# Optimization experiments

Hardware: AMD Instinct MI355X
Metric: run time of the kernel (lower is better)

The kernel has to match this reference:

```python
import jax, jax.numpy as jnp
import numpy as np

B, CQ, CKV, H, W = 4, 128, 256, 64, 64
NUM_HEADS = 8
SCALE = (CQ // NUM_HEADS) ** (-0.5)


def setup_inputs() -> dict:
    key = jax.random.key(0)
    ks = jax.random.split(key, 10)
    s = 0.02
    return {
        "x_q": jax.random.normal(ks[0], (B, CQ, H, W), dtype=jnp.float32),
        "x_kv": jax.random.normal(ks[1], (B, CKV, H, W), dtype=jnp.float32),
        "Wq": jax.random.normal(ks[2], (CQ, CQ), dtype=jnp.float32) * s,
        "bq": jnp.zeros((CQ,), dtype=jnp.float32),
        "Wk": jax.random.normal(ks[3], (CQ, CKV), dtype=jnp.float32) * s,
        "bk": jnp.zeros((CQ,), dtype=jnp.float32),
        "Wv": jax.random.normal(ks[4], (CQ, CKV), dtype=jnp.float32) * s,
        "bv": jnp.zeros((CQ,), dtype=jnp.float32),
        "Wo": jax.random.normal(ks[5], (CQ, CQ), dtype=jnp.float32) * s,
        "bo": jnp.zeros((CQ,), dtype=jnp.float32),
    }


def _conv1x1(x, Wm, bv_):
    # 1x1 conv == channel-mixing matmul: [B,C,H,W] x [O,C] -> [B,O,H,W]
    return jnp.einsum('bchw,oc->bohw', x, Wm) + bv_[:, None, None]


def reference(x_q, x_kv, Wq, bq, Wk, bk, Wv, bv, Wo, bo):
    b, c, h, w = x_q.shape
    n = h * w
    Q = _conv1x1(x_q, Wq, bq).reshape(b, c, n)   # [B,C,N]
    K = _conv1x1(x_kv, Wk, bk).reshape(b, c, n)  # [B,C,N]
    V = _conv1x1(x_kv, Wv, bv).reshape(b, c, n)  # [B,C,N]
    # attn = softmax(Q^T K * scale) over keys: [B,N,N]
    attn = jax.nn.softmax(jnp.einsum('bcn,bcm->bnm', Q, K) * SCALE, axis=-1)
    out = jnp.einsum('bnm,bcm->bcn', attn, V).reshape(b, c, h, w)
    out = _conv1x1(out, Wo, bo) + x_q
    return out
```

## Files before the change

### kernel.cpp

```cpp
#include <hip/hip_runtime.h>
#include <hip/hip_bf16.h>

typedef __bf16 bf16x8 __attribute__((ext_vector_type(8)));
typedef float f32x4 __attribute__((ext_vector_type(4)));
typedef float f32x16 __attribute__((ext_vector_type(16)));

#define MFMA16(a, b, c) __builtin_amdgcn_mfma_f32_16x16x32_bf16(a, b, c, 0, 0, 0)
#define MFMA32(a, b, c) __builtin_amdgcn_mfma_f32_32x32x16_bf16(a, b, c, 0, 0, 0)

static constexpr int NSP = 4096;
static constexpr float SCALE_L2E = 0.25f * 1.4426950408889634f;

__device__ __forceinline__ bf16x8 ld_frag(const void* p) {
  int4 v = *(const int4*)p;
  return __builtin_bit_cast(bf16x8, v);
}

__device__ __forceinline__ unsigned pk2(float a, float b) {
  unsigned short x = __builtin_bit_cast(unsigned short, (__bf16)a);
  unsigned short y = __builtin_bit_cast(unsigned short, (__bf16)b);
  return (unsigned)x | ((unsigned)y << 16);
}

__device__ __forceinline__ void load_lds16(const void* g, void* l) {
  __builtin_amdgcn_global_load_lds(
      (const __attribute__((address_space(1))) unsigned*)g,
      (__attribute__((address_space(3))) unsigned*)l, 16, 0, 0);
}

__global__ void k_prep(const float* __restrict__ Wq, const float* __restrict__ bq,
                       const float* __restrict__ Wk, const float* __restrict__ Wv,
                       const float* __restrict__ Wo,
                       __bf16* __restrict__ wqb, __bf16* __restrict__ wkb,
                       __bf16* __restrict__ wvb, __bf16* __restrict__ wob,
                       float* __restrict__ bqs) {
  int i = blockIdx.x * 256 + threadIdx.x;
  if (i < 16384)      wqb[i]          = (__bf16)(Wq[i] * SCALE_L2E);
  else if (i < 49152) wkb[i - 16384]  = (__bf16)Wk[i - 16384];
  else if (i < 81920) wvb[i - 49152]  = (__bf16)Wv[i - 49152];
  else if (i < 98304) wob[i - 81920]  = (__bf16)Wo[i - 81920];
  if (i < 128) bqs[i] = bq[i] * SCALE_L2E;
}

template <bool SWZ>
__device__ __forceinline__ void store_tile_T(char* myt, const f32x4* acc, int g, int r,
                                             __bf16* dst_base) {
#pragma unroll
  for (int oc = 0; oc < 8; ++oc) {
#pragma unroll
    for (int rr = 0; rr < 4; ++rr) {
      int o = oc * 16 + g * 4 + rr;
      int byte = (r << 8) + (o << 1);
      byte ^= (r & 7) << 4;
      *(__bf16*)(myt + byte) = (__bf16)acc[oc][rr];
    }
  }
  int l = g * 16 + r;
#pragma unroll
  for (int p = 0; p < 4; ++p) {
    int u = p * 64 + l, row = u >> 4, seg = u & 15;
    int byte = (row << 8) + (seg << 4);
    if (!SWZ) byte ^= (row & 7) << 4;
    int4 v = *(int4*)(myt + byte);
    *(int4*)(dst_base + row * 128 + seg * 8) = v;
  }
}

__global__ __launch_bounds__(256) void k_proj(const float* __restrict__ xq,
                                              const float* __restrict__ xkv,
                                              const __bf16* __restrict__ wqb,
                                              const __bf16* __restrict__ wkb,
                                              const __bf16* __restrict__ wvb,
                                              const float* __restrict__ bqs,
                                              const float* __restrict__ bk,
                                              const float* __restrict__ bv,
                                              __bf16* __restrict__ Qt,
                                              __bf16* __restrict__ Kt,
                                              __bf16* __restrict__ Vm) {
  const int t = threadIdx.x, w = t >> 6, l = t & 63, r = l & 15, g = l >> 4;
  __shared__ __align__(16) char lds[16384];
  char* myt = lds + (w << 12);

  if (blockIdx.x < 256) {
    const int b = blockIdx.x >> 6;
    const int n0 = (blockIdx.x & 63) << 6;
    const int nl = n0 + (w << 4) + r;
    const float* xb = xq + ((size_t)b << 19);
    bf16x8 bx[4];
#pragma unroll
    for (int cc = 0; cc < 4; ++cc) {
#pragma unroll
      for (int i = 0; i < 8; ++i) {
        int c = cc * 32 + g * 8 + i;
        bx[cc][i] = (__bf16)xb[c * 4096 + nl];
      }
    }
    f32x4 acc[8];
#pragma unroll
    for (int oc = 0; oc < 8; ++oc)
#pragma unroll
      for (int rr = 0; rr < 4; ++rr) acc[oc][rr] = bqs[oc * 16 + g * 4 + rr];
#pragma unroll
    for (int oc = 0; oc < 8; ++oc) {
#pragma unroll
      for (int cc = 0; cc < 4; ++cc) {
        bf16x8 a = ld_frag(wqb + (oc * 16 + r) * 128 + cc * 32 + g * 8);
        acc[oc] = MFMA16(a, bx[cc], acc[oc]);
      }
    }
    store_tile_T<false>(myt, acc, g, r, Qt + ((size_t)(b * NSP + n0 + w * 16)) * 128);
  } else {
    const int bid = blockIdx.x - 256;
    const int b = bid >> 6;
    const int n0 = (bid & 63) << 6;
    const int nl = n0 + (w << 4) + r;
    const float* xb = xkv + ((size_t)b << 20);
    bf16x8 bx[8];
#pragma unroll
    for (int cc = 0; cc < 8; ++cc) {
#pragma unroll
      for (int i = 0; i < 8; ++i) {
        int c = cc * 32 + g * 8 + i;
        bx[cc][i] = (__bf16)xb[(size_t)c * 4096 + nl];
      }
    }
    f32x4 acc[8];
#pragma unroll
    for (int oc = 0; oc < 8; ++oc)
#pragma unroll
      for (int rr = 0; rr < 4; ++rr) acc[oc][rr] = bk[oc * 16 + g * 4 + rr];
#pragma unroll
    for (int oc = 0; oc < 8; ++oc) {
#pragma unroll
      for (int cc = 0; cc < 8; ++cc) {
        bf16x8 a = ld_frag(wkb + (oc * 16 + r) * 256 + cc * 32 + g * 8);
        acc[oc] = MFMA16(a, bx[cc], acc[oc]);
      }
    }
    store_tile_T<true>(myt, acc, g, r, Kt + ((size_t)(b * NSP + n0 + w * 16)) * 128);

    f32x4 av[8];
#pragma unroll
    for (int oc = 0; oc < 8; ++oc)
#pragma unroll
      for (int rr = 0; rr < 4; ++rr) av[oc][rr] = bv[oc * 16 + g * 4 + rr];
#pragma unroll
    for (int oc = 0; oc < 8; ++oc) {
#pragma unroll
      for (int cc = 0; cc < 8; ++cc) {
        bf16x8 a = ld_frag(wvb + (oc * 16 + r) * 256 + cc * 32 + g * 8);
        av[oc] = MFMA16(a, bx[cc], av[oc]);
      }
    }
#pragma unroll
    for (int oc = 0; oc < 8; ++oc) {
#pragma unroll
      for (int rr = 0; rr < 4; ++rr) {
        int o = oc * 16 + g * 4 + rr;
        Vm[((size_t)(b * 128 + o) << 12) + (nl ^ ((o & 3) << 3))] = (__bf16)av[oc][rr];
      }
    }
  }
}

template <int SPLIT>
__global__ __launch_bounds__(256, 3) void k_flash(const __bf16* __restrict__ Qt,
                                                  const __bf16* __restrict__ Kt,
                                                  const __bf16* __restrict__ Vm,
                                                  __bf16* __restrict__ Op,
                                                  float2* __restrict__ Ml) {
  const int bid = blockIdx.x;
  const int combo = bid & (4 * SPLIT - 1), qtile = bid / (4 * SPLIT);
  const int b = combo & 3, ks = combo >> 2;
  const int q0 = qtile << 7;
  const int NK = NSP / SPLIT;
  const int t = threadIdx.x, w = t >> 6, l = t & 63;
  const int q31 = l & 31, hi = l >> 5;
  const int swz = (q31 & 7) << 4;
  const int swzV = (q31 & 3) << 4;

  __shared__ __align__(16) char kl[2][8192];
  __shared__ __align__(16) char vl[2][8192];

  const int qA = q0 + w * 32 + q31;
  const __bf16* qp = Qt + ((size_t)(b * NSP + qA)) * 128;
  bf16x8 qf[8];
#pragma unroll
  for (int cc = 0; cc < 8; ++cc) qf[cc] = ld_frag(qp + cc * 16 + hi * 8);

  f32x16 acc[4];
#pragma unroll
  for (int c = 0; c < 4; ++c)
#pragma unroll
    for (int i = 0; i < 16; ++i) acc[c][i] = 0.f;
  f32x4 lp = (f32x4){0.f, 0.f, 0.f, 0.f};

  const char* kbase = (const char*)(Kt + ((size_t)(b * NSP) + ks * NK) * 128);
  const char* vbase = (const char*)(Vm + (size_t)b * 128 * NSP + ks * NK);

  auto STAGE = [&](int bi, int tt) {
#pragma unroll
    for (int i = 0; i < 2; ++i) {
      int u = i * 256 + t;
      load_lds16(kbase + tt * 8192 + u * 16, &kl[bi][u * 16]);
    }
#pragma unroll
    for (int i = 0; i < 2; ++i) {
      int u = i * 256 + t, ch = u >> 2, ko = u & 3;
      load_lds16(vbase + (size_t)ch * 8192 + tt * 64 + ko * 16, &vl[bi][u * 16]);
    }
  };

  STAGE(0, 0);
  __syncthreads();

  const int nit = NK / 32;
  for (int it = 0; it < nit; ++it) {
    const int cur = it & 1;
    if (it + 1 < nit) STAGE(cur ^ 1, it + 1);

    const char* kt = kl[cur];
    f32x16 s = {};
    __builtin_amdgcn_s_setprio(1);
#pragma unroll
    for (int cc = 0; cc < 8; ++cc) {
      bf16x8 kf = ld_frag(kt + (q31 << 8) + ((cc * 32 + hi * 16) ^ swz));
      s = MFMA32(kf, qf[cc], s);
    }
    __builtin_amdgcn_s_setprio(0);

#pragma unroll
    for (int i = 0; i < 16; ++i) s[i] = exp2f(s[i]);
#pragma unroll
    for (int i = 0; i < 16; ++i) lp[i & 3] += s[i];

    unsigned pA[4][2], rA[4][2];
#pragma unroll
    for (int q4 = 0; q4 < 4; ++q4) {
      pA[q4][0] = pk2(s[4 * q4 + 0], s[4 * q4 + 1]);
      pA[q4][1] = pk2(s[4 * q4 + 2], s[4 * q4 + 3]);
    }
#pragma unroll
    for (int q4 = 0; q4 < 4; ++q4) {
      rA[q4][0] = __shfl_xor(pA[q4][0], 32);
      rA[q4][1] = __shfl_xor(pA[q4][1], 32);
    }

    const char* vt = vl[cur];
    __builtin_amdgcn_s_setprio(1);
#pragma unroll
    for (int kb = 0; kb < 2; ++kb) {
      uint4 fa;
      fa.x = hi ? rA[2 * kb + 1][0] : pA[2 * kb][0];
      fa.y = hi ? rA[2 * kb + 1][1] : pA[2 * kb][1];
      fa.z = hi ? pA[2 * kb + 1][0] : rA[2 * kb][0];
      fa.w = hi ? pA[2 * kb + 1][1] : rA[2 * kb][1];
      bf16x8 pf = __builtin_bit_cast(bf16x8, fa);
#pragma unroll
      for (int cht = 0; cht < 4; ++cht) {
        bf16x8 vf = ld_frag(vt + (cht * 32 + q31) * 64 + ((kb * 32 + hi * 16) ^ swzV));
        acc[cht] = MFMA32(vf, pf, acc[cht]);
      }
    }
    __builtin_amdgcn_s_setprio(0);
    __syncthreads();
  }

  float lsum = (lp[0] + lp[1]) + (lp[2] + lp[3]);
  lsum += __shfl_xor(lsum, 32);

  const size_t rowA = (size_t)((ks * 4 + b) * NSP + qA) * 128;
#pragma unroll
  for (int cht = 0; cht < 4; ++cht) {
#pragma unroll
    for (int qq = 0; qq < 4; ++qq) {
      uint2 va;
      va.x = pk2(acc[cht][4 * qq + 0], acc[cht][4 * qq + 1]);
      va.y = pk2(acc[cht][4 * qq + 2], acc[cht][4 * qq + 3]);
      *(uint2*)(Op + rowA + cht * 32 + qq * 8 + hi * 4) = va;
    }
  }
  if (hi == 0) {
    Ml[(size_t)(ks * 4 + b) * NSP + qA] = make_float2(0.f, lsum);
  }
}

template <int SPLIT>
__global__ __launch_bounds__(256) void k_oproj(const __bf16* __restrict__ Op,
                                               const float2* __restrict__ Ml,
                                               const __bf16* __restrict__ wob,
                                               const float* __restrict__ bo,
                                               const float* __restrict__ xq,
                                               float* __restrict__ out) {
  const int b = blockIdx.x >> 6;
  const int n0 = (blockIdx.x & 63) << 6;
  const int t = threadIdx.x, w = t >> 6, l = t & 63, r = l & 15, g = l >> 4;
  const int nl = n0 + (w << 4) + r;

  float den = 0.f;
#pragma unroll
  for (int s = 0; s < SPLIT; ++s) den += Ml[(size_t)(s * 4 + b) * NSP + nl].y;
  float inv = 1.f / den;

  bf16x8 bfr[4];
#pragma unroll
  for (int cc = 0; cc < 4; ++cc) {
    float a8[8];
#pragma unroll
    for (int j = 0; j < 8; ++j) a8[j] = 0.f;
#pragma unroll
    for (int s = 0; s < SPLIT; ++s) {
      bf16x8 a = ld_frag(Op + ((size_t)(s * 4 + b) * NSP + nl) * 128 + cc * 32 + g * 8);
#pragma unroll
      for (int j = 0; j < 8; ++j) a8[j] += (float)a[j];
    }
#pragma unroll
    for (int j = 0; j < 8; ++j) bfr[cc][j] = (__bf16)(a8[j] * inv);
  }

  f32x4 acc[8];
#pragma unroll
  for (int oc = 0; oc < 8; ++oc)
#pragma unroll
    for (int rr = 0; rr < 4; ++rr) acc[oc][rr] = bo[oc * 16 + g * 4 + rr];
#pragma unroll
  for (int oc = 0; oc < 8; ++oc) {
#pragma unroll
    for (int cc = 0; cc < 4; ++cc) {
      bf16x8 a = ld_frag(wob + (oc * 16 + r) * 128 + cc * 32 + g * 8);
      acc[oc] = MFMA16(a, bfr[cc], acc[oc]);
    }
  }
#pragma unroll
  for (int oc = 0; oc < 8; ++oc) {
#pragma unroll
    for (int rr = 0; rr < 4; ++rr) {
      int o = oc * 16 + g * 4 + rr;
      size_t idx = ((size_t)(b * 128 + o) << 12) + nl;
      out[idx] = acc[oc][rr] + xq[idx];
    }
  }
}

extern "C" void kernel_launch(void* const* d_in, const int* in_sizes, int n_in,
                              void* d_out, int out_size, void* d_ws, size_t ws_size,
                              hipStream_t stream) {
  const float* xq = (const float*)d_in[0];
  const float* xkv = (const float*)d_in[1];
  const float* Wq = (const float*)d_in[2];
  const float* bq = (const float*)d_in[3];
  const float* Wk = (const float*)d_in[4];
  const float* bk = (const float*)d_in[5];
  const float* Wv = (const float*)d_in[6];
  const float* bv = (const float*)d_in[7];
  const float* Wo = (const float*)d_in[8];
  const float* bo = (const float*)d_in[9];
  float* out = (float*)d_out;

  char* ws = (char*)d_ws;
  __bf16* wqb = (__bf16*)(ws);
  __bf16* wkb = (__bf16*)(ws + 32768);
  __bf16* wvb = (__bf16*)(ws + 98304);
  __bf16* wob = (__bf16*)(ws + 163840);
  float* bqs = (float*)(ws + 196608);
  __bf16* Qt = (__bf16*)(ws + 197120);
  __bf16* Kt = (__bf16*)(ws + 197120 + 4194304);
  __bf16* Vm = (__bf16*)(ws + 197120 + 2 * 4194304);
  __bf16* Op = (__bf16*)(ws + 197120 + 3 * 4194304);
  float2* Ml = (float2*)(ws + 197120 + 3 * 4194304 + 33554432);

  k_prep<<<dim3(384), dim3(256), 0, stream>>>(Wq, bq, Wk, Wv, Wo, wqb, wkb, wvb, wob, bqs);
  k_proj<<<dim3(512), dim3(256), 0, stream>>>(xq, xkv, wqb, wkb, wvb, bqs, bk, bv,
                                              Qt, Kt, Vm);

  const size_t base = 197120ull + 3ull * 4194304;
  const size_t need8 = base + 33554432ull + 1048576ull;
  const size_t need4 = base + 16777216ull + 524288ull;
  if (ws_size >= need8) {
    k_flash<8><<<dim3(1024), dim3(256), 0, stream>>>(Qt, Kt, Vm, Op, Ml);
    k_oproj<8><<<dim3(256), dim3(256), 0, stream>>>(Op, Ml, wob, bo, xq, out);
  } else if (ws_size >= need4) {
    float2* Ml4 = (float2*)(ws + base + 16777216);
    k_flash<4><<<dim3(512), dim3(256), 0, stream>>>(Qt, Kt, Vm, Op, Ml4);
    k_oproj<4><<<dim3(256), dim3(256), 0, stream>>>(Op, Ml4, wob, bo, xq, out);
  } else {
    float2* Ml2 = (float2*)(ws + base + 8388608);
    k_flash<2><<<dim3(256), dim3(256), 0, stream>>>(Qt, Kt, Vm, Op, Ml2);
    k_oproj<2><<<dim3(256), dim3(256), 0, stream>>>(Op, Ml2, wob, bo, xq, out);
  }
}
```

Baseline: 103.0 us.

## Restructure flash loop with explicit barriers, permlane swap, split MFMA chains, new swizzles

Reworks the flash-attention inner loop. It unrolls by two with compile-time buffer indices and replaces __syncthreads with explicit s_barrier plus vmcnt waits so the next K/V tile's loads stay in flight. The QK^T MFMA chain is split into two independent accumulators to shorten the dependency chain. The P-fragment exchange now uses permlane32_swap instead of shuffles and selects, and the softmax denominator is accumulated as a vector add. The K and V LDS swizzle patterns are changed to cut bank conflicts, with matching changes on the producer side. This adds register pressure and relies on manual waitcnt correctness, and the unrolled loop assumes an even iteration count.

Result: slower. 113.0 us (+9.7%).

```diff
diff --git a/kernel.cpp b/kernel.cpp
--- a/kernel.cpp
+++ b/kernel.cpp
@@ -4,9 +4,16 @@
 typedef __bf16 bf16x8 __attribute__((ext_vector_type(8)));
 typedef float f32x4 __attribute__((ext_vector_type(4)));
 typedef float f32x16 __attribute__((ext_vector_type(16)));
+typedef unsigned u32x2 __attribute__((ext_vector_type(2)));
 
 #define MFMA16(a, b, c) __builtin_amdgcn_mfma_f32_16x16x32_bf16(a, b, c, 0, 0, 0)
 #define MFMA32(a, b, c) __builtin_amdgcn_mfma_f32_32x32x16_bf16(a, b, c, 0, 0, 0)
+
+#if defined(__has_builtin)
+#if __has_builtin(__builtin_amdgcn_permlane32_swap)
+#define HAVE_PL32 1
+#endif
+#endif
 
 static constexpr int NSP = 4096;
 static constexpr float SCALE_L2E = 0.25f * 1.4426950408889634f;
@@ -50,8 +57,7 @@
 #pragma unroll
     for (int rr = 0; rr < 4; ++rr) {
       int o = oc * 16 + g * 4 + rr;
-      int byte = (r << 8) + (o << 1);
-      byte ^= (r & 7) << 4;
+      int byte = (r << 8) + (((o << 1)) ^ (r << 4));
       *(__bf16*)(myt + byte) = (__bf16)acc[oc][rr];
     }
   }
@@ -60,7 +66,7 @@
   for (int p = 0; p < 4; ++p) {
     int u = p * 64 + l, row = u >> 4, seg = u & 15;
     int byte = (row << 8) + (seg << 4);
-    if (!SWZ) byte ^= (row & 7) << 4;
+    if (!SWZ) byte ^= (row & 15) << 4;
     int4 v = *(int4*)(myt + byte);
     *(int4*)(dst_base + row * 128 + seg * 8) = v;
   }
@@ -157,7 +163,7 @@
 #pragma unroll
       for (int rr = 0; rr < 4; ++rr) {
         int o = oc * 16 + g * 4 + rr;
-        Vm[((size_t)(b * 128 + o) << 12) + (nl ^ ((o & 3) << 3))] = (__bf16)av[oc][rr];
+        Vm[((size_t)(b * 128 + o) << 12) + (nl ^ (((o >> 1) & 3) << 3))] = (__bf16)av[oc][rr];
       }
     }
   }
@@ -176,8 +182,8 @@
   const int NK = NSP / SPLIT;
   const int t = threadIdx.x, w = t >> 6, l = t & 63;
   const int q31 = l & 31, hi = l >> 5;
-  const int swz = (q31 & 7) << 4;
-  const int swzV = (q31 & 3) << 4;
+  const int swz = (q31 & 15) << 4;
+  const int swzV = ((q31 >> 1) & 3) << 4;
 
   __shared__ __align__(16) char kl[2][8192];
   __shared__ __align__(16) char vl[2][8192];
@@ -193,7 +199,7 @@
   for (int c = 0; c < 4; ++c)
 #pragma unroll
     for (int i = 0; i < 16; ++i) acc[c][i] = 0.f;
-  f32x4 lp = (f32x4){0.f, 0.f, 0.f, 0.f};
+  f32x16 lacc = {};
 
   const char* kbase = (const char*)(Kt + ((size_t)(b * NSP) + ks * NK) * 128);
   const char* vbase = (const char*)(Vm + (size_t)b * 128 * NSP + ks * NK);
@@ -212,61 +218,95 @@
   };
 
   STAGE(0, 0);
-  __syncthreads();
 
   const int nit = NK / 32;
-  for (int it = 0; it < nit; ++it) {
-    const int cur = it & 1;
-    if (it + 1 < nit) STAGE(cur ^ 1, it + 1);
-
-    const char* kt = kl[cur];
-    f32x16 s = {};
-    __builtin_amdgcn_s_setprio(1);
-#pragma unroll
-    for (int cc = 0; cc < 8; ++cc) {
-      bf16x8 kf = ld_frag(kt + (q31 << 8) + ((cc * 32 + hi * 16) ^ swz));
-      s = MFMA32(kf, qf[cc], s);
-    }
-    __builtin_amdgcn_s_setprio(0);
-
-#pragma unroll
-    for (int i = 0; i < 16; ++i) s[i] = exp2f(s[i]);
-#pragma unroll
-    for (int i = 0; i < 16; ++i) lp[i & 3] += s[i];
-
-    unsigned pA[4][2], rA[4][2];
-#pragma unroll
-    for (int q4 = 0; q4 < 4; ++q4) {
-      pA[q4][0] = pk2(s[4 * q4 + 0], s[4 * q4 + 1]);
-      pA[q4][1] = pk2(s[4 * q4 + 2], s[4 * q4 + 3]);
-    }
-#pragma unroll
-    for (int q4 = 0; q4 < 4; ++q4) {
-      rA[q4][0] = __shfl_xor(pA[q4][0], 32);
-      rA[q4][1] = __shfl_xor(pA[q4][1], 32);
-    }
-
-    const char* vt = vl[cur];
-    __builtin_amdgcn_s_setprio(1);
-#pragma unroll
-    for (int kb = 0; kb < 2; ++kb) {
-      uint4 fa;
-      fa.x = hi ? rA[2 * kb + 1][0] : pA[2 * kb][0];
-      fa.y = hi ? rA[2 * kb + 1][1] : pA[2 * kb][1];
-      fa.z = hi ? pA[2 * kb + 1][0] : rA[2 * kb][0];
-      fa.w = hi ? pA[2 * kb + 1][1] : rA[2 * kb][1];
-      bf16x8 pf = __builtin_bit_cast(bf16x8, fa);
-#pragma unroll
-      for (int cht = 0; cht < 4; ++cht) {
-        bf16x8 vf = ld_frag(vt + (cht * 32 + q31) * 64 + ((kb * 32 + hi * 16) ^ swzV));
-        acc[cht] = MFMA32(vf, pf, acc[cht]);
-      }
-    }
-    __builtin_amdgcn_s_setprio(0);
-    __syncthreads();
-  }
-
-  float lsum = (lp[0] + lp[1]) + (lp[2] + lp[3]);
+
+#define FLASH_BODY(CUR, IT)                                                    \
+  {                                                                            \
+    asm volatile("s_barrier" ::: "memory");                                    \
+    if ((IT) + 1 < nit) {                                                      \
+      STAGE((CUR) ^ 1, (IT) + 1);                                              \
+      asm volatile("s_waitcnt vmcnt(4)" ::: "memory");                         \
+    } else {                                                                   \
+      asm volatile("s_waitcnt vmcnt(0)" ::: "memory");                         \
+    }                                                                          \
+    __builtin_amdgcn_sched_barrier(0);                                         \
+    asm volatile("s_barrier" ::: "memory");                                    \
+    const char* kt = kl[CUR];                                                  \
+    f32x16 sX = {}, sY = {};                                                   \
+    __builtin_amdgcn_s_setprio(1);                                             \
+    _Pragma("unroll") for (int cc = 0; cc < 4; ++cc) {                         \
+      bf16x8 kf0 = ld_frag(kt + (q31 << 8) + ((cc * 32 + hi * 16) ^ swz));     \
+      bf16x8 kf1 = ld_frag(kt + (q31 << 8) + (((cc + 4) * 32 + hi * 16) ^ swz)); \
+      sX = MFMA32(kf0, qf[cc], sX);                                            \
+      sY = MFMA32(kf1, qf[cc + 4], sY);                                        \
+    }                                                                          \
+    __builtin_amdgcn_s_setprio(0);                                             \
+    f32x16 s = sX + sY;                                                        \
+    _Pragma("unroll") for (int i = 0; i < 16; ++i) s[i] = exp2f(s[i]);         \
+    lacc += s;                                                                 \
+    unsigned pA[4][2];                                                         \
+    _Pragma("unroll") for (int q4 = 0; q4 < 4; ++q4) {                         \
+      pA[q4][0] = pk2(s[4 * q4 + 0], s[4 * q4 + 1]);                           \
+      pA[q4][1] = pk2(s[4 * q4 + 2], s[4 * q4 + 3]);                           \
+    }                                                                          \
+    uint4 pfA4, pfB4;                                                          \
+    EXCHANGE_P                                                                 \
+    const char* vt = vl[CUR];                                                  \
+    bf16x8 pfA = __builtin_bit_cast(bf16x8, pfA4);                             \
+    bf16x8 pfB = __builtin_bit_cast(bf16x8, pfB4);                             \
+    __builtin_amdgcn_s_setprio(1);                                             \
+    _Pragma("unroll") for (int cht = 0; cht < 4; ++cht) {                      \
+      bf16x8 vf0 = ld_frag(vt + (cht * 32 + q31) * 64 + ((hi * 16) ^ swzV));   \
+      bf16x8 vf1 = ld_frag(vt + (cht * 32 + q31) * 64 + ((32 + hi * 16) ^ swzV)); \
+      acc[cht] = MFMA32(vf0, pfA, acc[cht]);                                   \
+      acc[cht] = MFMA32(vf1, pfB, acc[cht]);                                   \
+    }                                                                          \
+    __builtin_amdgcn_s_setprio(0);                                             \
+  }
+
+#ifdef HAVE_PL32
+#define EXCHANGE_P                                                             \
+  {                                                                            \
+    u32x2 r_;                                                                  \
+    r_ = __builtin_amdgcn_permlane32_swap(pA[0][0], pA[1][0], false, false);   \
+    pfA4.x = r_[0]; pfA4.z = r_[1];                                            \
+    r_ = __builtin_amdgcn_permlane32_swap(pA[0][1], pA[1][1], false, false);   \
+    pfA4.y = r_[0]; pfA4.w = r_[1];                                            \
+    r_ = __builtin_amdgcn_permlane32_swap(pA[2][0], pA[3][0], false, false);   \
+    pfB4.x = r_[0]; pfB4.z = r_[1];                                            \
+    r_ = __builtin_amdgcn_permlane32_swap(pA[2][1], pA[3][1], false, false);   \
+    pfB4.y = r_[0]; pfB4.w = r_[1];                                            \
+  }
+#else
+#define EXCHANGE_P                                                             \
+  {                                                                            \
+    unsigned rA[4][2];                                                         \
+    _Pragma("unroll") for (int q4 = 0; q4 < 4; ++q4) {                         \
+      rA[q4][0] = __shfl_xor(pA[q4][0], 32);                                   \
+      rA[q4][1] = __shfl_xor(pA[q4][1], 32);                                   \
+    }                                                                          \
+    pfA4.x = hi ? rA[1][0] : pA[0][0];                                         \
+    pfA4.y = hi ? rA[1][1] : pA[0][1];                                         \
+    pfA4.z = hi ? pA[1][0] : rA[0][0];                                         \
+    pfA4.w = hi ? pA[1][1] : rA[0][1];                                         \
+    pfB4.x = hi ? rA[3][0] : pA[2][0];                                         \
+    pfB4.y = hi ? rA[3][1] : pA[2][1];                                         \
+    pfB4.z = hi ? pA[3][0] : rA[2][0];                                         \
+    pfB4.w = hi ? pA[3][1] : rA[2][1];                                         \
+  }
+#endif
+
+  for (int it = 0; it < nit; it += 2) {
+    FLASH_BODY(0, it)
+    FLASH_BODY(1, it + 1)
+  }
+#undef FLASH_BODY
+#undef EXCHANGE_P
+
+  float lsum = 0.f;
+#pragma unroll
+  for (int i = 0; i < 16; ++i) lsum += lacc[i];
   lsum += __shfl_xor(lsum, 32);
 
   const size_t rowA = (size_t)((ks * 4 + b) * NSP + qA) * 128;
```
